# Performance work log

Measured on AMD Instinct MI355X. Metric: run time of the kernel, lower is better.

Reference implementation:

```python
import jax, jax.numpy as jnp
import numpy as np

B, N = 64, 512
D_ENT, H = 2000, 768
LN_EPS = 1e-12


def setup_inputs() -> dict:
    key = jax.random.key(0)
    ks = jax.random.split(key, 16)
    s = 1.0 / np.sqrt(D_ENT)
    sh = 1.0 / np.sqrt(H)
    return {
        "node_embeddings": jax.random.normal(ks[0], (B, N, D_ENT), jnp.float32),
        "node_types": jax.random.randint(ks[1], (B, N), 0, 2),
        "layers": jax.random.randint(ks[2], (B, N), 0, 8),
        "operators": jax.random.randint(ks[3], (B, N), 0, 2),
        "in_degs": jax.random.randint(ks[4], (B, N), 0, 8),
        "out_degs": jax.random.randint(ks[5], (B, N), 0, 8),
        "negs": jax.random.randint(ks[6], (B, N), 0, 2),
        "type_emb": jax.random.normal(ks[7], (2, H), jnp.float32),
        "layer_emb": jax.random.normal(ks[8], (8, H), jnp.float32),
        "op_emb": jax.random.normal(ks[9], (2, H), jnp.float32),
        "in_emb": jax.random.normal(ks[10], (8, H), jnp.float32),
        "out_emb": jax.random.normal(ks[11], (8, H), jnp.float32),
        "proj_w": jax.random.uniform(ks[12], (H, D_ENT), jnp.float32, -s, s),
        "proj_b": jnp.zeros((H,), jnp.float32),
        "neg_w": jax.random.uniform(ks[13], (H, H), jnp.float32, -sh, sh),
        "neg_b": jnp.zeros((H,), jnp.float32),
        "ln_g": jnp.ones((H,), jnp.float32),
        "ln_b": jnp.zeros((H,), jnp.float32),
    }


def reference(node_embeddings, node_types, layers, operators, in_degs, out_degs, negs,
              type_emb, layer_emb, op_emb, in_emb, out_emb,
              proj_w, proj_b, neg_w, neg_b, ln_g, ln_b):
    # linear projection: [B,N,D_ENT] @ [D_ENT,H]
    x = jnp.einsum("bnd,hd->bnh", node_embeddings, proj_w) + proj_b
    # summed small-table lookups
    x = x + type_emb[node_types] + layer_emb[layers] + op_emb[operators] \
        + in_emb[in_degs] + out_emb[out_degs]
    # rows with negs==1 go through MLP (single Linear h->h); masked select/scatter
    y = jnp.einsum("bnh,gh->bng", x, neg_w) + neg_b
    x = jnp.where((negs == 1)[..., None], y, x)
    # LayerNorm
    mu = jnp.mean(x, axis=-1, keepdims=True)
    var = jnp.mean(jnp.square(x - mu), axis=-1, keepdims=True)
    x = (x - mu) * jax.lax.rsqrt(var + LN_EPS) * ln_g + ln_b
    # dropout is identity in eval mode
    return x
```

## Files before the change

### kernel.cpp

```cpp
#include <hip/hip_runtime.h>
#include <stdint.h>

typedef unsigned short u16;
typedef short v8s __attribute__((ext_vector_type(8)));
typedef float v4f __attribute__((ext_vector_type(4)));

typedef __attribute__((address_space(1))) uint32_t g_u32;
typedef __attribute__((address_space(3))) uint32_t l_u32;

__device__ __forceinline__ void glds16(const void* g, void* l) {
    __builtin_amdgcn_global_load_lds((const g_u32*)g, (l_u32*)l, 16, 0, 0);
}

__device__ __forceinline__ u16 f2b(float f) {
    uint32_t u = __builtin_bit_cast(uint32_t, f);
    u += 0x7FFFu + ((u >> 16) & 1u);
    return (u16)(u >> 16);
}

__device__ __forceinline__ uint32_t pk2(float a, float b) {
    uint32_t ua = __builtin_bit_cast(uint32_t, a) + 0x8000u;
    uint32_t ub = __builtin_bit_cast(uint32_t, b) + 0x8000u;
    return __builtin_amdgcn_perm(ub, ua, 0x07060302u);
}

#define MTOT  32768
#define HDIM  768
#define KDIM  2000
#define KPAD  2016

__global__ __launch_bounds__(256) void cvt_weights(
    const float* __restrict__ pw, const float* __restrict__ nw,
    u16* __restrict__ Wb, u16* __restrict__ NWb)
{
    const int h = blockIdx.x;
    const float* src = pw + (size_t)h * KDIM;
    u16* dst = Wb + (size_t)h * KPAD;
    for (int k = threadIdx.x; k < KPAD; k += 256)
        dst[k] = (k < KDIM) ? f2b(src[k]) : (u16)0;
    const float* s2 = nw + (size_t)h * HDIM;
    u16* d2 = NWb + (size_t)h * HDIM;
    for (int k = threadIdx.x; k < HDIM; k += 256)
        d2[k] = f2b(s2[k]);
}

__global__ __launch_bounds__(256, 3) void gemm1(
    const float* __restrict__ A, const u16* __restrict__ Wb,
    const float* __restrict__ pb,
    const int* __restrict__ i_ty, const int* __restrict__ i_la,
    const int* __restrict__ i_op, const int* __restrict__ i_in, const int* __restrict__ i_ou,
    const float* __restrict__ te, const float* __restrict__ le, const float* __restrict__ oe,
    const float* __restrict__ ie, const float* __restrict__ ooe,
    u16* __restrict__ Xb)
{
    __shared__ __align__(16) float Asf[128 * 32];
    __shared__ __align__(16) u16  Bs[128 * 32];

    const int bid = blockIdx.x;
    const int slot = bid >> 3;
    const int mt = (bid & 7) * 32 + slot / 6;
    const int nt = slot % 6;
    const int m_base = mt * 128, n_base = nt * 128;

    const int tid = threadIdx.x;
    const int w = tid >> 6, lane = tid & 63;
    const int lm = lane & 15, quad = lane >> 4;
    const int wm = (w >> 1) * 64, wn = (w & 1) * 64;

    const float* aRowBase[4];
    int aChunkOff[4];
    float* aDst[4];
#pragma unroll
    for (int t = 0; t < 4; t++) {
        const int rl = w * 32 + t * 8 + (lane >> 3);
        const int c16 = (lane & 7) ^ (rl & 7);
        aRowBase[t] = A + (size_t)(m_base + rl) * KDIM;
        aChunkOff[t] = c16 * 4;
        aDst[t] = &Asf[(w * 32 + t * 8) * 32];
    }
    const u16* bSrc[2];
    u16* bDst[2];
#pragma unroll
    for (int t = 0; t < 2; t++) {
        const int rl = w * 32 + t * 16 + (lane >> 2);
        const int c = (lane & 3) ^ ((rl >> 1) & 3);
        bSrc[t] = Wb + (size_t)(n_base + rl) * KPAD + c * 8;
        bDst[t] = &Bs[(w * 32 + t * 16) * 32];
    }

    v4f acc[4][4];
#pragma unroll
    for (int i = 0; i < 4; i++)
#pragma unroll
        for (int j = 0; j < 4; j++) acc[i][j] = (v4f){0.f, 0.f, 0.f, 0.f};

    for (int kb = 0; kb < KPAD / 32; ++kb) {
        __syncthreads();
#pragma unroll
        for (int t = 0; t < 4; t++) {
            int k = kb * 32 + aChunkOff[t];
            k = (k > 1996) ? 1996 : k;
            glds16(aRowBase[t] + k, aDst[t]);
        }
#pragma unroll
        for (int t = 0; t < 2; t++)
            glds16(bSrc[t] + kb * 32, bDst[t]);
        __syncthreads();

        v8s af[4], bf[4];
#pragma unroll
        for (int i = 0; i < 4; i++) {
            const int r = wm + i * 16 + lm;
            const int sw = r & 7;
            const float4 lo = *(const float4*)&Asf[r * 32 + (((2 * quad)     ^ sw) << 2)];
            const float4 hi = *(const float4*)&Asf[r * 32 + (((2 * quad + 1) ^ sw) << 2)];
            int4 p;
            p.x = (int)pk2(lo.x, lo.y); p.y = (int)pk2(lo.z, lo.w);
            p.z = (int)pk2(hi.x, hi.y); p.w = (int)pk2(hi.z, hi.w);
            af[i] = __builtin_bit_cast(v8s, p);
        }
#pragma unroll
        for (int j = 0; j < 4; j++) {
            const int r = wn + j * 16 + lm;
            bf[j] = *(const v8s*)&Bs[r * 32 + (quad ^ ((r >> 1) & 3)) * 8];
        }
#pragma unroll
        for (int i = 0; i < 4; i++)
#pragma unroll
            for (int j = 0; j < 4; j++)
                acc[i][j] = __builtin_amdgcn_mfma_f32_16x16x32_bf16(af[i], bf[j], acc[i][j], 0, 0, 0);
    }

#pragma unroll
    for (int i = 0; i < 4; i++) {
#pragma unroll
        for (int r = 0; r < 4; r++) {
            const int row = m_base + wm + i * 16 + quad * 4 + r;
            const int ty = i_ty[row], la = i_la[row], op = i_op[row];
            const int di = i_in[row], doo = i_ou[row];
            const float* pte = te + (size_t)ty * HDIM;
            const float* ple = le + (size_t)la * HDIM;
            const float* poe = oe + (size_t)op * HDIM;
            const float* pie = ie + (size_t)di * HDIM;
            const float* pou = ooe + (size_t)doo * HDIM;
            u16* orow = Xb + (size_t)row * HDIM;
#pragma unroll
            for (int j = 0; j < 4; j++) {
                const int col = n_base + wn + j * 16 + lm;
                float v = acc[i][j][r] + pb[col] + pte[col] + ple[col] + poe[col] + pie[col] + pou[col];
                orow[col] = f2b(v);
            }
        }
    }
}

__global__ __launch_bounds__(256, 3) void gemm2(
    const u16* __restrict__ Xb, const u16* __restrict__ NWb,
    const float* __restrict__ nb, u16* __restrict__ Yb)
{
    __shared__ __align__(16) u16 As[128 * 32];
    __shared__ __align__(16) u16 Bs[128 * 32];

    const int bid = blockIdx.x;
    const int slot = bid >> 3;
    const int mt = (bid & 7) * 32 + slot / 6;
    const int nt = slot % 6;
    const int m_base = mt * 128, n_base = nt * 128;

    const int tid = threadIdx.x;
    const int w = tid >> 6, lane = tid & 63;
    const int lm = lane & 15, quad = lane >> 4;
    const int wm = (w >> 1) * 64, wn = (w & 1) * 64;

    const u16* aSrc[2]; u16* aDst[2];
    const u16* bSrc[2]; u16* bDst[2];
#pragma unroll
    for (int t = 0; t < 2; t++) {
        const int rl = w * 32 + t * 16 + (lane >> 2);
        const int c = (lane & 3) ^ ((rl >> 1) & 3);
        aSrc[t] = Xb  + (size_t)(m_base + rl) * HDIM + c * 8;
        aDst[t] = &As[(w * 32 + t * 16) * 32];
        bSrc[t] = NWb + (size_t)(n_base + rl) * HDIM + c * 8;
        bDst[t] = &Bs[(w * 32 + t * 16) * 32];
    }

    v4f acc[4][4];
#pragma unroll
    for (int i = 0; i < 4; i++)
#pragma unroll
        for (int j = 0; j < 4; j++) acc[i][j] = (v4f){0.f, 0.f, 0.f, 0.f};

    for (int kb = 0; kb < HDIM / 32; ++kb) {
        __syncthreads();
#pragma unroll
        for (int t = 0; t < 2; t++) {
            glds16(aSrc[t] + kb * 32, aDst[t]);
            glds16(bSrc[t] + kb * 32, bDst[t]);
        }
        __syncthreads();

        v8s af[4], bf[4];
#pragma unroll
        for (int i = 0; i < 4; i++) {
            const int r = wm + i * 16 + lm;
            af[i] = *(const v8s*)&As[r * 32 + (quad ^ ((r >> 1) & 3)) * 8];
        }
#pragma unroll
        for (int j = 0; j < 4; j++) {
            const int r = wn + j * 16 + lm;
            bf[j] = *(const v8s*)&Bs[r * 32 + (quad ^ ((r >> 1) & 3)) * 8];
        }
#pragma unroll
        for (int i = 0; i < 4; i++)
#pragma unroll
            for (int j = 0; j < 4; j++)
                acc[i][j] = __builtin_amdgcn_mfma_f32_16x16x32_bf16(af[i], bf[j], acc[i][j], 0, 0, 0);
    }

#pragma unroll
    for (int i = 0; i < 4; i++) {
#pragma unroll
        for (int r = 0; r < 4; r++) {
            const int row = m_base + wm + i * 16 + quad * 4 + r;
            u16* orow = Yb + (size_t)row * HDIM;
#pragma unroll
            for (int j = 0; j < 4; j++) {
                const int col = n_base + wn + j * 16 + lm;
                orow[col] = f2b(acc[i][j][r] + nb[col]);
            }
        }
    }
}

__global__ __launch_bounds__(256) void ln_k(
    const u16* __restrict__ Xb, const u16* __restrict__ Yb,
    const int* __restrict__ negs,
    const float* __restrict__ g, const float* __restrict__ b,
    float* __restrict__ out)
{
    const int w = threadIdx.x >> 6, lane = threadIdx.x & 63;
    const int row = blockIdx.x * 4 + w;
    const u16* src = ((negs[row] == 1) ? Yb : Xb) + (size_t)row * HDIM;

    float v[12];
    float s = 0.f, ss = 0.f;
#pragma unroll
    for (int p = 0; p < 3; p++) {
        uint2 u = *(const uint2*)(src + (p * 64 + lane) * 4);
        float f0 = __builtin_bit_cast(float, u.x << 16);
        float f1 = __builtin_bit_cast(float, u.x & 0xFFFF0000u);
        float f2 = __builtin_bit_cast(float, u.y << 16);
        float f3 = __builtin_bit_cast(float, u.y & 0xFFFF0000u);
        v[p * 4 + 0] = f0; v[p * 4 + 1] = f1; v[p * 4 + 2] = f2; v[p * 4 + 3] = f3;
        s += f0 + f1 + f2 + f3;
        ss += f0 * f0 + f1 * f1 + f2 * f2 + f3 * f3;
    }
#pragma unroll
    for (int off = 1; off < 64; off <<= 1) {
        s += __shfl_xor(s, off);
        ss += __shfl_xor(ss, off);
    }
    const float mean = s * (1.f / (float)HDIM);
    const float var = ss * (1.f / (float)HDIM) - mean * mean;
    const float rs = rsqrtf(var + 1e-12f);

    float* orow = out + (size_t)row * HDIM;
#pragma unroll
    for (int p = 0; p < 3; p++) {
        const int c0 = (p * 64 + lane) * 4;
        float4 gg = *(const float4*)(g + c0);
        float4 bb = *(const float4*)(b + c0);
        float4 o;
        o.x = (v[p * 4 + 0] - mean) * rs * gg.x + bb.x;
        o.y = (v[p * 4 + 1] - mean) * rs * gg.y + bb.y;
        o.z = (v[p * 4 + 2] - mean) * rs * gg.z + bb.z;
        o.w = (v[p * 4 + 3] - mean) * rs * gg.w + bb.w;
        *(float4*)(orow + c0) = o;
    }
}

extern "C" void kernel_launch(void* const* d_in, const int* in_sizes, int n_in,
                              void* d_out, int out_size, void* d_ws, size_t ws_size,
                              hipStream_t stream) {
    (void)in_sizes; (void)n_in; (void)out_size; (void)ws_size;
    const float* A   = (const float*)d_in[0];
    const int* i_ty  = (const int*)d_in[1];
    const int* i_la  = (const int*)d_in[2];
    const int* i_op  = (const int*)d_in[3];
    const int* i_in  = (const int*)d_in[4];
    const int* i_ou  = (const int*)d_in[5];
    const int* negs  = (const int*)d_in[6];
    const float* te  = (const float*)d_in[7];
    const float* le  = (const float*)d_in[8];
    const float* oe  = (const float*)d_in[9];
    const float* ie  = (const float*)d_in[10];
    const float* ooe = (const float*)d_in[11];
    const float* pw  = (const float*)d_in[12];
    const float* pb  = (const float*)d_in[13];
    const float* nw  = (const float*)d_in[14];
    const float* nb  = (const float*)d_in[15];
    const float* lng = (const float*)d_in[16];
    const float* lnb = (const float*)d_in[17];
    float* out = (float*)d_out;

    char* ws = (char*)d_ws;
    u16* Wb  = (u16*)ws;
    u16* NWb = (u16*)(ws + 3096576);
    u16* Xb  = (u16*)(ws + 3096576 + 1179648);
    u16* Yb  = (u16*)(ws + 3096576 + 1179648 + 50331648);

    cvt_weights<<<768, 256, 0, stream>>>(pw, nw, Wb, NWb);
    gemm1<<<1536, 256, 0, stream>>>(A, Wb, pb, i_ty, i_la, i_op, i_in, i_ou,
                                    te, le, oe, ie, ooe, Xb);
    gemm2<<<1536, 256, 0, stream>>>(Xb, NWb, nb, Yb);
    ln_k<<<8192, 256, 0, stream>>>(Xb, Yb, negs, lng, lnb, out);
}
```

Before: 677.4 us.

## Double-buffer LDS in both GEMMs and convert A to bf16 before storing

Both GEMM kernels now use two LDS buffers, so the next K-tile is fetched while MFMAs run on the current one. This removes one of the two barriers per iteration. In gemm1 the fp32 A tile is loaded into registers, packed to bf16 once, and written to LDS. Previously fp32 went to LDS and was converted on every fragment read. The change adds register pressure from the in-flight A loads and doubles the LDS buffers, which may affect occupancy at 3 blocks per CU.

```diff
diff --git a/kernel.cpp b/kernel.cpp
--- a/kernel.cpp
+++ b/kernel.cpp
@@ -53,8 +53,8 @@
     const float* __restrict__ ie, const float* __restrict__ ooe,
     u16* __restrict__ Xb)
 {
-    __shared__ __align__(16) float Asf[128 * 32];
-    __shared__ __align__(16) u16  Bs[128 * 32];
+    __shared__ __align__(16) u16 As[2][128 * 32];
+    __shared__ __align__(16) u16 Bs[2][128 * 32];
 
     const int bid = blockIdx.x;
     const int slot = bid >> 3;
@@ -67,25 +67,24 @@
     const int lm = lane & 15, quad = lane >> 4;
     const int wm = (w >> 1) * 64, wn = (w & 1) * 64;
 
-    const float* aRowBase[4];
-    int aChunkOff[4];
-    float* aDst[4];
-#pragma unroll
-    for (int t = 0; t < 4; t++) {
-        const int rl = w * 32 + t * 8 + (lane >> 3);
-        const int c16 = (lane & 7) ^ (rl & 7);
-        aRowBase[t] = A + (size_t)(m_base + rl) * KDIM;
-        aChunkOff[t] = c16 * 4;
-        aDst[t] = &Asf[(w * 32 + t * 8) * 32];
+    const float* aRow[2];
+    int aOff[2];
+    int aLds[2];
+#pragma unroll
+    for (int t = 0; t < 2; t++) {
+        const int rl = w * 32 + t * 16 + (lane >> 2);
+        aRow[t] = A + (size_t)(m_base + rl) * KDIM;
+        aOff[t] = ((lane & 3) ^ ((rl >> 1) & 3)) << 3;
+        aLds[t] = rl * 32 + ((lane & 3) << 3);
     }
     const u16* bSrc[2];
-    u16* bDst[2];
+    int bLds[2];
 #pragma unroll
     for (int t = 0; t < 2; t++) {
         const int rl = w * 32 + t * 16 + (lane >> 2);
         const int c = (lane & 3) ^ ((rl >> 1) & 3);
         bSrc[t] = Wb + (size_t)(n_base + rl) * KPAD + c * 8;
-        bDst[t] = &Bs[(w * 32 + t * 16) * 32];
+        bLds[t] = (w * 32 + t * 16) * 32;
     }
 
     v4f acc[4][4];
@@ -94,35 +93,80 @@
 #pragma unroll
         for (int j = 0; j < 4; j++) acc[i][j] = (v4f){0.f, 0.f, 0.f, 0.f};
 
-    for (int kb = 0; kb < KPAD / 32; ++kb) {
-        __syncthreads();
-#pragma unroll
-        for (int t = 0; t < 4; t++) {
-            int k = kb * 32 + aChunkOff[t];
-            k = (k > 1996) ? 1996 : k;
-            glds16(aRowBase[t] + k, aDst[t]);
+    {
+        float4 a0[2], a1[2];
+#pragma unroll
+        for (int t = 0; t < 2; t++) {
+            const int kf = aOff[t];
+            a0[t] = *(const float4*)(aRow[t] + kf);
+            a1[t] = *(const float4*)(aRow[t] + kf + 4);
         }
 #pragma unroll
         for (int t = 0; t < 2; t++)
-            glds16(bSrc[t] + kb * 32, bDst[t]);
-        __syncthreads();
+            glds16(bSrc[t], &Bs[0][bLds[t]]);
+#pragma unroll
+        for (int t = 0; t < 2; t++) {
+            int4 p;
+            p.x = (int)pk2(a0[t].x, a0[t].y); p.y = (int)pk2(a0[t].z, a0[t].w);
+            p.z = (int)pk2(a1[t].x, a1[t].y); p.w = (int)pk2(a1[t].z, a1[t].w);
+            *(v8s*)&As[0][aLds[t]] = __builtin_bit_cast(v8s, p);
+        }
+    }
+    __syncthreads();
+
+    int cur = 0;
+#pragma unroll 2
+    for (int kb = 0; kb < KPAD / 32 - 1; ++kb) {
+        float4 a0[2], a1[2];
+#pragma unroll
+        for (int t = 0; t < 2; t++) {
+            int kf = (kb + 1) * 32 + aOff[t];
+            kf = (kf > 1992) ? 1992 : kf;
+            a0[t] = *(const float4*)(aRow[t] + kf);
+            a1[t] = *(const float4*)(aRow[t] + kf + 4);
+        }
+#pragma unroll
+        for (int t = 0; t < 2; t++)
+            glds16(bSrc[t] + (kb + 1) * 32, &Bs[cur ^ 1][bLds[t]]);
 
         v8s af[4], bf[4];
 #pragma unroll
         for (int i = 0; i < 4; i++) {
             const int r = wm + i * 16 + lm;
-            const int sw = r & 7;
-            const float4 lo = *(const float4*)&Asf[r * 32 + (((2 * quad)     ^ sw) << 2)];
-            const float4 hi = *(const float4*)&Asf[r * 32 + (((2 * quad + 1) ^ sw) << 2)];
-            int4 p;
-            p.x = (int)pk2(lo.x, lo.y); p.y = (int)pk2(lo.z, lo.w);
-            p.z = (int)pk2(hi.x, hi.y); p.w = (int)pk2(hi.z, hi.w);
-            af[i] = __builtin_bit_cast(v8s, p);
+            af[i] = *(const v8s*)&As[cur][r * 32 + ((quad ^ ((r >> 1) & 3)) << 3)];
         }
 #pragma unroll
         for (int j = 0; j < 4; j++) {
             const int r = wn + j * 16 + lm;
-            bf[j] = *(const v8s*)&Bs[r * 32 + (quad ^ ((r >> 1) & 3)) * 8];
+            bf[j] = *(const v8s*)&Bs[cur][r * 32 + ((quad ^ ((r >> 1) & 3)) << 3)];
+        }
+#pragma unroll
+        for (int i = 0; i < 4; i++)
+#pragma unroll
+            for (int j = 0; j < 4; j++)
+                acc[i][j] = __builtin_amdgcn_mfma_f32_16x16x32_bf16(af[i], bf[j], acc[i][j], 0, 0, 0);
+
+#pragma unroll
+        for (int t = 0; t < 2; t++) {
+            int4 p;
+            p.x = (int)pk2(a0[t].x, a0[t].y); p.y = (int)pk2(a0[t].z, a0[t].w);
+            p.z = (int)pk2(a1[t].x, a1[t].y); p.w = (int)pk2(a1[t].z, a1[t].w);
+            *(v8s*)&As[cur ^ 1][aLds[t]] = __builtin_bit_cast(v8s, p);
+        }
+        __syncthreads();
+        cur ^= 1;
+    }
+    {
+        v8s af[4], bf[4];
+#pragma unroll
+        for (int i = 0; i < 4; i++) {
+            const int r = wm + i * 16 + lm;
+            af[i] = *(const v8s*)&As[cur][r * 32 + ((quad ^ ((r >> 1) & 3)) << 3)];
+        }
+#pragma unroll
+        for (int j = 0; j < 4; j++) {
+            const int r = wn + j * 16 + lm;
+            bf[j] = *(const v8s*)&Bs[cur][r * 32 + ((quad ^ ((r >> 1) & 3)) << 3)];
         }
 #pragma unroll
         for (int i = 0; i < 4; i++)
@@ -158,8 +202,8 @@
     const u16* __restrict__ Xb, const u16* __restrict__ NWb,
     const float* __restrict__ nb, u16* __restrict__ Yb)
 {
-    __shared__ __align__(16) u16 As[128 * 32];
-    __shared__ __align__(16) u16 Bs[128 * 32];
+    __shared__ __align__(16) u16 As[2][128 * 32];
+    __shared__ __align__(16) u16 Bs[2][128 * 32];
 
     const int bid = blockIdx.x;
     const int slot = bid >> 3;
@@ -172,16 +216,16 @@
     const int lm = lane & 15, quad = lane >> 4;
     const int wm = (w >> 1) * 64, wn = (w & 1) * 64;
 
-    const u16* aSrc[2]; u16* aDst[2];
-    const u16* bSrc[2]; u16* bDst[2];
+    const u16* aSrc[2];
+    const u16* bSrc[2];
+    int sLds[2];
 #pragma unroll
     for (int t = 0; t < 2; t++) {
         const int rl = w * 32 + t * 16 + (lane >> 2);
         const int c = (lane & 3) ^ ((rl >> 1) & 3);
         aSrc[t] = Xb  + (size_t)(m_base + rl) * HDIM + c * 8;
-        aDst[t] = &As[(w * 32 + t * 16) * 32];
         bSrc[t] = NWb + (size_t)(n_base + rl) * HDIM + c * 8;
-        bDst[t] = &Bs[(w * 32 + t * 16) * 32];
+        sLds[t] = (w * 32 + t * 16) * 32;
     }
 
     v4f acc[4][4];
@@ -190,25 +234,53 @@
 #pragma unroll
         for (int j = 0; j < 4; j++) acc[i][j] = (v4f){0.f, 0.f, 0.f, 0.f};
 
-    for (int kb = 0; kb < HDIM / 32; ++kb) {
-        __syncthreads();
-#pragma unroll
-        for (int t = 0; t < 2; t++) {
-            glds16(aSrc[t] + kb * 32, aDst[t]);
-            glds16(bSrc[t] + kb * 32, bDst[t]);
-        }
-        __syncthreads();
+#pragma unroll
+    for (int t = 0; t < 2; t++) {
+        glds16(aSrc[t], &As[0][sLds[t]]);
+        glds16(bSrc[t], &Bs[0][sLds[t]]);
+    }
+    __syncthreads();
+
+    int cur = 0;
+#pragma unroll 2
+    for (int kb = 0; kb < HDIM / 32 - 1; ++kb) {
+#pragma unroll
+        for (int t = 0; t < 2; t++) {
+            glds16(aSrc[t] + (kb + 1) * 32, &As[cur ^ 1][sLds[t]]);
+            glds16(bSrc[t] + (kb + 1) * 32, &Bs[cur ^ 1][sLds[t]]);
+        }
 
         v8s af[4], bf[4];
 #pragma unroll
         for (int i = 0; i < 4; i++) {
             const int r = wm + i * 16 + lm;
-            af[i] = *(const v8s*)&As[r * 32 + (quad ^ ((r >> 1) & 3)) * 8];
+            af[i] = *(const v8s*)&As[cur][r * 32 + ((quad ^ ((r >> 1) & 3)) << 3)];
         }
 #pragma unroll
         for (int j = 0; j < 4; j++) {
             const int r = wn + j * 16 + lm;
-            bf[j] = *(const v8s*)&Bs[r * 32 + (quad ^ ((r >> 1) & 3)) * 8];
+            bf[j] = *(const v8s*)&Bs[cur][r * 32 + ((quad ^ ((r >> 1) & 3)) << 3)];
+        }
+#pragma unroll
+        for (int i = 0; i < 4; i++)
+#pragma unroll
+            for (int j = 0; j < 4; j++)
+                acc[i][j] = __builtin_amdgcn_mfma_f32_16x16x32_bf16(af[i], bf[j], acc[i][j], 0, 0, 0);
+
+        __syncthreads();
+        cur ^= 1;
+    }
+    {
+        v8s af[4], bf[4];
+#pragma unroll
+        for (int i = 0; i < 4; i++) {
+            const int r = wm + i * 16 + lm;
+            af[i] = *(const v8s*)&As[cur][r * 32 + ((quad ^ ((r >> 1) & 3)) << 3)];
+        }
+#pragma unroll
+        for (int j = 0; j < 4; j++) {
+            const int r = wn + j * 16 + lm;
+            bf[j] = *(const v8s*)&Bs[cur][r * 32 + ((quad ^ ((r >> 1) & 3)) << 3)];
         }
 #pragma unroll
         for (int i = 0; i < 4; i++)
```

New measurement: 681.5 us. Within noise of the previous version (+0.6%).

## Triple-buffer LDS tiles in both GEMMs with async prefetch pipeline

Applied to the files above, without the earlier changes.

Both GEMM kernels now keep three shared-memory stages and issue global-to-LDS loads two K-steps ahead. A single barrier per step is guarded by explicit vmcnt waits, replacing the earlier pair of syncthreads per step that left no overlap between loads and MFMA work. This hides memory latency behind compute. In exchange it triples LDS use, and gemm1's occupancy hint drops from 3 to 2 blocks per CU. The hand-coded waitcnt counts assume a fixed number of outstanding loads per stage.

```diff
diff --git a/kernel.cpp b/kernel.cpp
--- a/kernel.cpp
+++ b/kernel.cpp
@@ -44,7 +44,7 @@
         d2[k] = f2b(s2[k]);
 }
 
-__global__ __launch_bounds__(256, 3) void gemm1(
+__global__ __launch_bounds__(256, 2) void gemm1(
     const float* __restrict__ A, const u16* __restrict__ Wb,
     const float* __restrict__ pb,
     const int* __restrict__ i_ty, const int* __restrict__ i_la,
@@ -53,8 +53,8 @@
     const float* __restrict__ ie, const float* __restrict__ ooe,
     u16* __restrict__ Xb)
 {
-    __shared__ __align__(16) float Asf[128 * 32];
-    __shared__ __align__(16) u16  Bs[128 * 32];
+    __shared__ __align__(16) float Asf[3][128 * 32];
+    __shared__ __align__(16) u16  Bs[3][128 * 32];
 
     const int bid = blockIdx.x;
     const int slot = bid >> 3;
@@ -68,24 +68,24 @@
     const int wm = (w >> 1) * 64, wn = (w & 1) * 64;
 
     const float* aRowBase[4];
-    int aChunkOff[4];
-    float* aDst[4];
+    int aOff[4];
+    int aBase[4];
 #pragma unroll
     for (int t = 0; t < 4; t++) {
         const int rl = w * 32 + t * 8 + (lane >> 3);
         const int c16 = (lane & 7) ^ (rl & 7);
         aRowBase[t] = A + (size_t)(m_base + rl) * KDIM;
-        aChunkOff[t] = c16 * 4;
-        aDst[t] = &Asf[(w * 32 + t * 8) * 32];
+        aOff[t] = c16 * 4;
+        aBase[t] = (w * 32 + t * 8) * 32;
     }
     const u16* bSrc[2];
-    u16* bDst[2];
+    int bBase[2];
 #pragma unroll
     for (int t = 0; t < 2; t++) {
         const int rl = w * 32 + t * 16 + (lane >> 2);
         const int c = (lane & 3) ^ ((rl >> 1) & 3);
         bSrc[t] = Wb + (size_t)(n_base + rl) * KPAD + c * 8;
-        bDst[t] = &Bs[(w * 32 + t * 16) * 32];
+        bBase[t] = (w * 32 + t * 16) * 32;
     }
 
     v4f acc[4][4];
@@ -94,26 +94,28 @@
 #pragma unroll
         for (int j = 0; j < 4; j++) acc[i][j] = (v4f){0.f, 0.f, 0.f, 0.f};
 
-    for (int kb = 0; kb < KPAD / 32; ++kb) {
-        __syncthreads();
+    auto issue = [&](int kb) {
+        const int sl = kb % 3;
 #pragma unroll
         for (int t = 0; t < 4; t++) {
-            int k = kb * 32 + aChunkOff[t];
+            int k = kb * 32 + aOff[t];
             k = (k > 1996) ? 1996 : k;
-            glds16(aRowBase[t] + k, aDst[t]);
+            glds16(aRowBase[t] + k, &Asf[sl][aBase[t]]);
         }
 #pragma unroll
         for (int t = 0; t < 2; t++)
-            glds16(bSrc[t] + kb * 32, bDst[t]);
-        __syncthreads();
-
+            glds16(bSrc[t] + kb * 32, &Bs[sl][bBase[t]]);
+    };
+
+    auto compute = [&](int kb) {
+        const int sl = kb % 3;
         v8s af[4], bf[4];
 #pragma unroll
         for (int i = 0; i < 4; i++) {
             const int r = wm + i * 16 + lm;
             const int sw = r & 7;
-            const float4 lo = *(const float4*)&Asf[r * 32 + (((2 * quad)     ^ sw) << 2)];
-            const float4 hi = *(const float4*)&Asf[r * 32 + (((2 * quad + 1) ^ sw) << 2)];
+            const float4 lo = *(const float4*)&Asf[sl][r * 32 + (((2 * quad)     ^ sw) << 2)];
+            const float4 hi = *(const float4*)&Asf[sl][r * 32 + (((2 * quad + 1) ^ sw) << 2)];
             int4 p;
             p.x = (int)pk2(lo.x, lo.y); p.y = (int)pk2(lo.z, lo.w);
             p.z = (int)pk2(hi.x, hi.y); p.w = (int)pk2(hi.z, hi.w);
@@ -122,14 +124,33 @@
 #pragma unroll
         for (int j = 0; j < 4; j++) {
             const int r = wn + j * 16 + lm;
-            bf[j] = *(const v8s*)&Bs[r * 32 + (quad ^ ((r >> 1) & 3)) * 8];
+            bf[j] = *(const v8s*)&Bs[sl][r * 32 + ((quad ^ ((r >> 1) & 3)) << 3)];
         }
 #pragma unroll
         for (int i = 0; i < 4; i++)
 #pragma unroll
             for (int j = 0; j < 4; j++)
                 acc[i][j] = __builtin_amdgcn_mfma_f32_16x16x32_bf16(af[i], bf[j], acc[i][j], 0, 0, 0);
-    }
+    };
+
+    issue(0);
+    issue(1);
+
+    for (int kb = 0; kb < 61; ++kb) {
+        asm volatile("s_waitcnt vmcnt(6)" ::: "memory");
+        __builtin_amdgcn_s_barrier();
+        __builtin_amdgcn_sched_barrier(0);
+        issue(kb + 2);
+        compute(kb);
+    }
+    asm volatile("s_waitcnt vmcnt(6)" ::: "memory");
+    __builtin_amdgcn_s_barrier();
+    __builtin_amdgcn_sched_barrier(0);
+    compute(61);
+    asm volatile("s_waitcnt vmcnt(0)" ::: "memory");
+    __builtin_amdgcn_s_barrier();
+    __builtin_amdgcn_sched_barrier(0);
+    compute(62);
 
 #pragma unroll
     for (int i = 0; i < 4; i++) {
@@ -158,8 +179,8 @@
     const u16* __restrict__ Xb, const u16* __restrict__ NWb,
     const float* __restrict__ nb, u16* __restrict__ Yb)
 {
-    __shared__ __align__(16) u16 As[128 * 32];
-    __shared__ __align__(16) u16 Bs[128 * 32];
+    __shared__ __align__(16) u16 As[3][128 * 32];
+    __shared__ __align__(16) u16 Bs[3][128 * 32];
 
     const int bid = blockIdx.x;
     const int slot = bid >> 3;
@@ -172,16 +193,16 @@
     const int lm = lane & 15, quad = lane >> 4;
     const int wm = (w >> 1) * 64, wn = (w & 1) * 64;
 
-    const u16* aSrc[2]; u16* aDst[2];
-    const u16* bSrc[2]; u16* bDst[2];
+    const u16* aSrc[2];
+    const u16* bSrc[2];
+    int sBase[2];
 #pragma unroll
     for (int t = 0; t < 2; t++) {
         const int rl = w * 32 + t * 16 + (lane >> 2);
         const int c = (lane & 3) ^ ((rl >> 1) & 3);
         aSrc[t] = Xb  + (size_t)(m_base + rl) * HDIM + c * 8;
-        aDst[t] = &As[(w * 32 + t * 16) * 32];
         bSrc[t] = NWb + (size_t)(n_base + rl) * HDIM + c * 8;
-        bDst[t] = &Bs[(w * 32 + t * 16) * 32];
+        sBase[t] = (w * 32 + t * 16) * 32;
     }
 
     v4f acc[4][4];
@@ -190,32 +211,53 @@
 #pragma unroll
         for (int j = 0; j < 4; j++) acc[i][j] = (v4f){0.f, 0.f, 0.f, 0.f};
 
-    for (int kb = 0; kb < HDIM / 32; ++kb) {
-        __syncthreads();
+    auto issue = [&](int kb) {
+        const int sl = kb % 3;
 #pragma unroll
         for (int t = 0; t < 2; t++) {
-            glds16(aSrc[t] + kb * 32, aDst[t]);
-            glds16(bSrc[t] + kb * 32, bDst[t]);
-        }
-        __syncthreads();
-
+            glds16(aSrc[t] + kb * 32, &As[sl][sBase[t]]);
+            glds16(bSrc[t] + kb * 32, &Bs[sl][sBase[t]]);
+        }
+    };
+
+    auto compute = [&](int kb) {
+        const int sl = kb % 3;
         v8s af[4], bf[4];
 #pragma unroll
         for (int i = 0; i < 4; i++) {
             const int r = wm + i * 16 + lm;
-            af[i] = *(const v8s*)&As[r * 32 + (quad ^ ((r >> 1) & 3)) * 8];
+            af[i] = *(const v8s*)&As[sl][r * 32 + ((quad ^ ((r >> 1) & 3)) << 3)];
         }
 #pragma unroll
         for (int j = 0; j < 4; j++) {
             const int r = wn + j * 16 + lm;
-            bf[j] = *(const v8s*)&Bs[r * 32 + (quad ^ ((r >> 1) & 3)) * 8];
+            bf[j] = *(const v8s*)&Bs[sl][r * 32 + ((quad ^ ((r >> 1) & 3)) << 3)];
         }
 #pragma unroll
         for (int i = 0; i < 4; i++)
 #pragma unroll
             for (int j = 0; j < 4; j++)
                 acc[i][j] = __builtin_amdgcn_mfma_f32_16x16x32_bf16(af[i], bf[j], acc[i][j], 0, 0, 0);
-    }
+    };
+
+    issue(0);
+    issue(1);
+
+    for (int kb = 0; kb < 22; ++kb) {
+        asm volatile("s_waitcnt vmcnt(4)" ::: "memory");
+        __builtin_amdgcn_s_barrier();
+        __builtin_amdgcn_sched_barrier(0);
+        issue(kb + 2);
+        compute(kb);
+    }
+    asm volatile("s_waitcnt vmcnt(4)" ::: "memory");
+    __builtin_amdgcn_s_barrier();
+    __builtin_amdgcn_sched_barrier(0);
+    compute(22);
+    asm volatile("s_waitcnt vmcnt(0)" ::: "memory");
+    __builtin_amdgcn_s_barrier();
+    __builtin_amdgcn_sched_barrier(0);
+    compute(23);
 
 #pragma unroll
     for (int i = 0; i < 4; i++) {
```

Result: slower. 730.0 us (+7.8%).
